# Performance work log

Measured on AMD Instinct MI355X. Metric: run time of the kernel, lower is better.

Reference implementation:

```python
import jax, jax.numpy as jnp
import numpy as np

N_BINS = 15


def setup_inputs() -> dict:
    key = jax.random.key(0)
    k1, k2 = jax.random.split(key)
    probs = jax.random.uniform(k1, (1, 2, 4096, 4096), dtype=jnp.float32)
    labels = jax.random.randint(k2, (1, 1, 4096, 4096), 0, 2, dtype=jnp.int32)
    return {"probs": probs, "labels": labels}


def _bin_stats(conf, acc, boundaries):
    # bin i holds conf in (boundaries[i], boundaries[i+1]] -> searchsorted left - 1
    idx = jnp.searchsorted(boundaries, conf, side="left") - 1
    valid = (idx >= 0) & (idx < N_BINS)
    idx = jnp.where(valid, idx, N_BINS)  # route invalid (conf==0) to overflow bin
    vmask = valid.astype(conf.dtype)
    count = jax.ops.segment_sum(vmask, idx, num_segments=N_BINS + 1)[:N_BINS]
    csum = jax.ops.segment_sum(conf * vmask, idx, num_segments=N_BINS + 1)[:N_BINS]
    asum = jax.ops.segment_sum(acc * vmask, idx, num_segments=N_BINS + 1)[:N_BINS]
    return count, csum, asum


def reference(probs, labels):
    h, w = probs.shape[2], probs.shape[3]
    boundaries = jnp.linspace(0.0, 1.0, N_BINS + 1)
    conf0 = probs[0, 0].reshape(h * w)
    conf1 = probs[0, 1].reshape(h * w)
    lab = labels[0, 0].reshape(h * w)
    acc0 = (lab == 0).astype(probs.dtype)
    acc1 = (lab == 1).astype(probs.dtype)
    count0, csum0, asum0 = _bin_stats(conf0, acc0, boundaries)
    count1, csum1, asum1 = _bin_stats(conf1, acc1, boundaries)
    return (count0, csum0, asum0, count1, csum1, asum1)
```

## Files before the change

kernel.cpp:

```cpp
#include <hip/hip_runtime.h>
#include <stdint.h>


#define NBINS 15

__global__ void zero_out_kernel(float* out, int n) {
    int i = blockIdx.x * blockDim.x + threadIdx.x;
    if (i < n) out[i] = 0.0f;
}

__device__ __forceinline__ void bin_one(unsigned long long* h, float c, int match) {
    if (c > 0.0f && c <= 1.0f) {
        int bin = (int)(c * 15.0f);
        bin = bin > 14 ? 14 : bin;
        unsigned int cf = __float2uint_rn(c * 262144.0f);
        unsigned long long v = ((unsigned long long)cf << 32)
                             | ((unsigned long long)(match ? 1u : 0u) << 16)
                             | 1ull;
        atomicAdd(&h[bin], v);
    }
}

__global__ __launch_bounds__(256) void calib_hist_kernel(
        const float* __restrict__ probs, const int* __restrict__ labels,
        float* __restrict__ out, int npix) {
    __shared__ unsigned long long hist[16 * 33];
    int tid = threadIdx.x;
    for (int i = tid; i < 16 * 33; i += 256) hist[i] = 0ull;
    __syncthreads();

    unsigned long long* h = &hist[(tid >> 4) * 33];

    const float4* p0 = (const float4*)probs;
    const float4* p1 = (const float4*)(probs + npix);
    const int4*   lb = (const int4*)labels;
    int nvec   = npix >> 2;
    int stride = gridDim.x * blockDim.x;
    for (int i = blockIdx.x * blockDim.x + tid; i < nvec; i += stride) {
        float4 a = p0[i];
        float4 b = p1[i];
        int4   l = lb[i];
        bin_one(h,      a.x, l.x == 0);
        bin_one(h + 16, b.x, l.x == 1);
        bin_one(h,      a.y, l.y == 0);
        bin_one(h + 16, b.y, l.y == 1);
        bin_one(h,      a.z, l.z == 0);
        bin_one(h + 16, b.z, l.z == 1);
        bin_one(h,      a.w, l.w == 0);
        bin_one(h + 16, b.w, l.w == 1);
    }
    __syncthreads();

    if (tid < 2 * NBINS) {
        int ch = tid / NBINS, bin = tid % NBINS;
        unsigned long long cnt = 0, asum = 0, csum = 0;
        for (int wg = 0; wg < 16; ++wg) {
            unsigned long long x = hist[wg * 33 + ch * 16 + bin];
            cnt  += x & 0xFFFFull;
            asum += (x >> 16) & 0xFFFFull;
            csum += x >> 32;
        }
        float* base = out + ch * 45;
        atomicAdd(base + bin,            (float)cnt);
        atomicAdd(base + NBINS + bin,    (float)csum * (1.0f / 262144.0f));
        atomicAdd(base + 2 * NBINS + bin,(float)asum);
    }
}

extern "C" void kernel_launch(void* const* d_in, const int* in_sizes, int n_in,
                              void* d_out, int out_size, void* d_ws, size_t ws_size,
                              hipStream_t stream) {
    const float* probs  = (const float*)d_in[0];
    const int*   labels = (const int*)d_in[1];
    float*       out    = (float*)d_out;
    int npix = in_sizes[1];

    zero_out_kernel<<<(out_size + 127) / 128, 128, 0, stream>>>(out, out_size);

    calib_hist_kernel<<<2048, 256, 0, stream>>>(probs, labels, out, npix);
}
```

Before: 301.7 us.

## Replace shared-memory atomics with per-thread private histograms in LDS

```diff
diff --git a/kernel.cpp b/kernel.cpp
--- a/kernel.cpp
+++ b/kernel.cpp
@@ -9,61 +9,66 @@
     if (i < n) out[i] = 0.0f;
 }
 
-__device__ __forceinline__ void bin_one(unsigned long long* h, float c, int match) {
-    if (c > 0.0f && c <= 1.0f) {
-        int bin = (int)(c * 15.0f);
-        bin = bin > 14 ? 14 : bin;
-        unsigned int cf = __float2uint_rn(c * 262144.0f);
-        unsigned long long v = ((unsigned long long)cf << 32)
-                             | ((unsigned long long)(match ? 1u : 0u) << 16)
-                             | 1ull;
-        atomicAdd(&h[bin], v);
-    }
+__device__ __forceinline__ unsigned long long pack_update(float c, int match, int* bin_out) {
+    bool valid = (c > 0.0f) && (c <= 1.0f);
+    float cb = fmaxf(fminf(c * 15.0f, 14.0f), 0.0f);
+    *bin_out = (int)cb;
+    unsigned int cf = __float2uint_rn(fmaxf(c, 0.0f) * 262144.0f);
+    unsigned long long v = ((unsigned long long)cf << 32)
+                         | ((unsigned long long)(match ? 1u : 0u) << 16)
+                         | 1ull;
+    return valid ? v : 0ull;
 }
 
 __global__ __launch_bounds__(256) void calib_hist_kernel(
         const float* __restrict__ probs, const int* __restrict__ labels,
         float* __restrict__ out, int npix) {
-    __shared__ unsigned long long hist[16 * 33];
+    __shared__ unsigned long long hist[32 * 256];
     int tid = threadIdx.x;
-    for (int i = tid; i < 16 * 33; i += 256) hist[i] = 0ull;
+    #pragma unroll
+    for (int k = 0; k < 32; ++k) hist[k * 256 + tid] = 0ull;
     __syncthreads();
-
-    unsigned long long* h = &hist[(tid >> 4) * 33];
 
     const float4* p0 = (const float4*)probs;
     const float4* p1 = (const float4*)(probs + npix);
     const int4*   lb = (const int4*)labels;
     int nvec   = npix >> 2;
     int stride = gridDim.x * blockDim.x;
+
     for (int i = blockIdx.x * blockDim.x + tid; i < nvec; i += stride) {
         float4 a = p0[i];
         float4 b = p1[i];
         int4   l = lb[i];
-        bin_one(h,      a.x, l.x == 0);
-        bin_one(h + 16, b.x, l.x == 1);
-        bin_one(h,      a.y, l.y == 0);
-        bin_one(h + 16, b.y, l.y == 1);
-        bin_one(h,      a.z, l.z == 0);
-        bin_one(h + 16, b.z, l.z == 1);
-        bin_one(h,      a.w, l.w == 0);
-        bin_one(h + 16, b.w, l.w == 1);
+        int bin;
+        unsigned long long v;
+        v = pack_update(a.x, l.x == 0, &bin); hist[bin * 256 + tid] += v;
+        v = pack_update(b.x, l.x == 1, &bin); hist[(16 + bin) * 256 + tid] += v;
+        v = pack_update(a.y, l.y == 0, &bin); hist[bin * 256 + tid] += v;
+        v = pack_update(b.y, l.y == 1, &bin); hist[(16 + bin) * 256 + tid] += v;
+        v = pack_update(a.z, l.z == 0, &bin); hist[bin * 256 + tid] += v;
+        v = pack_update(b.z, l.z == 1, &bin); hist[(16 + bin) * 256 + tid] += v;
+        v = pack_update(a.w, l.w == 0, &bin); hist[bin * 256 + tid] += v;
+        v = pack_update(b.w, l.w == 1, &bin); hist[(16 + bin) * 256 + tid] += v;
     }
     __syncthreads();
 
-    if (tid < 2 * NBINS) {
-        int ch = tid / NBINS, bin = tid % NBINS;
+    if (tid < 32) {
+        int e = tid;
         unsigned long long cnt = 0, asum = 0, csum = 0;
-        for (int wg = 0; wg < 16; ++wg) {
-            unsigned long long x = hist[wg * 33 + ch * 16 + bin];
+        for (int it = 0; it < 256; ++it) {
+            int t = (it + e) & 255;
+            unsigned long long x = hist[e * 256 + t];
             cnt  += x & 0xFFFFull;
             asum += (x >> 16) & 0xFFFFull;
             csum += x >> 32;
         }
-        float* base = out + ch * 45;
-        atomicAdd(base + bin,            (float)cnt);
-        atomicAdd(base + NBINS + bin,    (float)csum * (1.0f / 262144.0f));
-        atomicAdd(base + 2 * NBINS + bin,(float)asum);
+        int ch = e >> 4, bin = e & 15;
+        if (bin < NBINS) {
+            float* base = out + ch * 45;
+            atomicAdd(base + bin,             (float)cnt);
+            atomicAdd(base + NBINS + bin,     (float)csum * (1.0f / 262144.0f));
+            atomicAdd(base + 2 * NBINS + bin, (float)asum);
+        }
     }
 }
 
@@ -77,5 +82,8 @@
 
     zero_out_kernel<<<(out_size + 127) / 128, 128, 0, stream>>>(out, out_size);
 
-    calib_hist_kernel<<<2048, 256, 0, stream>>>(probs, labels, out, npix);
+    int nvec = npix >> 2;
+    int blocks = (nvec + 256 * 32 - 1) / (256 * 32);
+    if (blocks < 1) blocks = 1;
+    calib_hist_kernel<<<blocks, 256, 0, stream>>>(probs, labels, out, npix);
 }
```

Result: faster. 258.1 us (-14.4%).
